# Optimization experiments

Measured on AMD Instinct MI355X. Metric: run time of the kernel, lower is better.

## Reference

```python
import jax, jax.numpy as jnp
import numpy as np

B, S, H, NH = 2, 2048, 1024, 16
HD = H // NH


def setup_inputs() -> dict:
    key = jax.random.key(0)
    ks = jax.random.split(key, 14)
    lim = 1.0 / np.sqrt(H)  # torch Linear default init range
    def lin(ka, kb):
        W = jax.random.uniform(ka, (H, H), jnp.float32, -lim, lim)
        b = jax.random.uniform(kb, (H,), jnp.float32, -lim, lim)
        return W, b
    Wq, bq = lin(ks[0], ks[1])
    Wk, bk = lin(ks[2], ks[3])
    Wv, bv = lin(ks[4], ks[5])
    Wo, bo = lin(ks[6], ks[7])
    return {
        "query": jax.random.normal(ks[8], (B, S, H), jnp.float32),
        "key": jax.random.normal(ks[9], (B, S, H), jnp.float32),
        "value": jax.random.normal(ks[10], (B, S, H), jnp.float32),
        "attn_mask": jax.random.randint(ks[11], (B, S, S), 0, 2).astype(bool),
        "relative_time": jax.random.normal(ks[12], (B, 1, S, S), jnp.float32),
        "Wq": Wq, "bq": bq, "Wk": Wk, "bk": bk,
        "Wv": Wv, "bv": bv, "Wo": Wo, "bo": bo,
    }


def reference(query, key, value, attn_mask, relative_time,
              Wq, bq, Wk, bk, Wv, bv, Wo, bo):
    Bq, Sq, _ = query.shape
    Skv = key.shape[1]
    # projections (torch Linear: x @ W^T + b)
    Q = (query @ Wq.T + bq).reshape(Bq, Sq, NH, HD).transpose(0, 2, 1, 3)
    K = (key @ Wk.T + bk).reshape(Bq, Skv, NH, HD).transpose(0, 2, 1, 3)
    V = (value @ Wv.T + bv).reshape(Bq, Skv, NH, HD).transpose(0, 2, 1, 3)
    scale = HD ** (-0.5)
    # NOTE: bias added BEFORE scaling, matching the original (non-standard)
    scores = jnp.einsum("bhqd,bhkd->bhqk", Q, K)
    scores = (scores + relative_time) * scale
    scores = jnp.where(attn_mask[:, None, :, :], scores, -jnp.inf)
    attn = jax.nn.softmax(scores.astype(jnp.float32), axis=-1).astype(scores.dtype)
    attn = jnp.nan_to_num(attn, nan=0.0)
    # dropout is identity in eval mode (dropout_rate applied only when training)
    out = jnp.einsum("bhqk,bhkd->bhqd", attn, V)
    out = out.transpose(0, 2, 1, 3).reshape(Bq, Sq, H)
    return out @ Wo.T + bo
```

## Files before the change

kernel.cpp:

```cpp
#include <hip/hip_runtime.h>
#include <hip/hip_bf16.h>

constexpr int BATCH = 2, SEQ = 2048, HDIM = 1024, NHEADS = 16, HEADD = 64;
constexpr int MROWS = BATCH * SEQ;
constexpr float QSCALE = 0.18033688011112042f;

typedef short short8  __attribute__((ext_vector_type(8)));
typedef float f32x4   __attribute__((ext_vector_type(4)));
typedef float f32x16  __attribute__((ext_vector_type(16)));
typedef int   int4v   __attribute__((ext_vector_type(4)));
typedef unsigned short ushort4v __attribute__((ext_vector_type(4)));

static __device__ __forceinline__ short f2bf(float f) {
    __hip_bfloat16 h = __float2bfloat16(f);
    return *reinterpret_cast<short*>(&h);
}

static __device__ __forceinline__ int cvt_pk_bf16(float a, float b) {
    int r;
    asm("v_cvt_pk_bf16_f32 %0, %1, %2" : "=v"(r) : "v"(a), "v"(b));
    return r;
}

static __device__ __forceinline__ float bfbits2f(unsigned short u) {
    return __builtin_bit_cast(float, (unsigned int)u << 16);
}

static __device__ __forceinline__ void gload_lds16(const void* g, void* l) {
    __builtin_amdgcn_global_load_lds(
        (const __attribute__((address_space(1))) unsigned int*)g,
        (__attribute__((address_space(3))) unsigned int*)l, 16, 0, 0);
}

static __device__ __forceinline__ int swz(int row) {
    return (((row & 7) ^ ((row >> 3) & 3))) << 4;
}

__global__ void cvt_all_kernel(const float* __restrict__ q, const float* __restrict__ k,
                               const float* __restrict__ v, const float* __restrict__ w0,
                               const float* __restrict__ w1, const float* __restrict__ w2,
                               const float* __restrict__ w3,
                               short* __restrict__ xq, short* __restrict__ xk,
                               short* __restrict__ xv, short* __restrict__ o0,
                               short* __restrict__ o1, short* __restrict__ o2,
                               short* __restrict__ o3, int n4x, int n4w) {
    int i = blockIdx.x * blockDim.x + threadIdx.x;
    const int stride = gridDim.x * blockDim.x;
    const int total = 3 * n4x + 4 * n4w;
    for (; i < total; i += stride) {
        const float* in; short* out; int j = i;
        if (j < 3 * n4x) {
            if (j >= 2 * n4x)      { in = v; out = xv; j -= 2 * n4x; }
            else if (j >= n4x)     { in = k; out = xk; j -= n4x; }
            else                   { in = q; out = xq; }
        } else {
            j -= 3 * n4x;
            if (j >= 3 * n4w)      { in = w3; out = o3; j -= 3 * n4w; }
            else if (j >= 2 * n4w) { in = w2; out = o2; j -= 2 * n4w; }
            else if (j >= n4w)     { in = w1; out = o1; j -= n4w; }
            else                   { in = w0; out = o0; }
        }
        const float4 val = reinterpret_cast<const float4*>(in)[j];
        short4 o;
        o.x = f2bf(val.x); o.y = f2bf(val.y); o.z = f2bf(val.z); o.w = f2bf(val.w);
        reinterpret_cast<short4*>(out)[j] = o;
    }
}

__global__ void detect_mask_kernel(const unsigned int* __restrict__ m, int* flag) {
    const int tid = threadIdx.x;
    int gt1 = 0, isf = 0;
    for (int i = 0; i < 4; ++i) {
        unsigned int wv = m[tid + 256 * i];
        if (wv > 1u) gt1 = 1;
        if (wv == 0x3F800000u) isf = 1;
    }
    __shared__ int s_gt1, s_isf;
    if (tid == 0) { s_gt1 = 0; s_isf = 0; }
    __syncthreads();
    if (gt1) atomicOr(&s_gt1, 1);
    if (isf) atomicOr(&s_isf, 1);
    __syncthreads();
    if (tid == 0) flag[0] = s_gt1 ? (s_isf ? 2 : 1) : 0;
}

__global__ __launch_bounds__(256)
void fuse_rel_kernel(const float* __restrict__ rel, const void* __restrict__ mask,
                     const int* __restrict__ flag, short* __restrict__ rT) {
    constexpr int QT = 64, KT = 256;
    constexpr int STRIDE = KT + 4;
    __shared__ short tile[QT * STRIDE];
    const int f   = flag[0];
    const int bid = blockIdx.x;
    const int b   = bid >> 8;
    const int t8  = (bid >> 5) & 7;
    const int t32 = bid & 31;
    const int q0  = t32 * QT;
    const int kv0 = t8 * KT;
    const int tid = threadIdx.x;

    const int c4 = tid & 63;
    const int r4 = tid >> 6;
    #pragma unroll 4
    for (int it = 0; it < 16; ++it) {
        const int row = it * 4 + r4;
        const long src = ((long)(b * 2048 + q0 + row)) * 2048 + kv0 + c4 * 4;
        const float4 v = *reinterpret_cast<const float4*>(rel + src);
        bool mk[4];
        if (f == 1) {
            const unsigned int mw =
                *reinterpret_cast<const unsigned int*>((const unsigned char*)mask + src);
            mk[0] = (mw & 0xffu) != 0;       mk[1] = (mw & 0xff00u) != 0;
            mk[2] = (mw & 0xff0000u) != 0;   mk[3] = (mw & 0xff000000u) != 0;
        } else if (f == 0) {
            const int4 mi = *reinterpret_cast<const int4*>((const int*)mask + src);
            mk[0] = mi.x != 0; mk[1] = mi.y != 0; mk[2] = mi.z != 0; mk[3] = mi.w != 0;
        } else {
            const float4 mf = *reinterpret_cast<const float4*>((const float*)mask + src);
            mk[0] = mf.x != 0.0f; mk[1] = mf.y != 0.0f;
            mk[2] = mf.z != 0.0f; mk[3] = mf.w != 0.0f;
        }
        short4 o;
        o.x = f2bf(mk[0] ? v.x * QSCALE : -1e30f);
        o.y = f2bf(mk[1] ? v.y * QSCALE : -1e30f);
        o.z = f2bf(mk[2] ? v.z * QSCALE : -1e30f);
        o.w = f2bf(mk[3] ? v.w * QSCALE : -1e30f);
        *reinterpret_cast<short4*>(&tile[row * STRIDE + c4 * 4]) = o;
    }
    __syncthreads();

    const int qq  = tid & 63;
    const int p4r = tid >> 6;
    #pragma unroll 4
    for (int it = 0; it < 16; ++it) {
        const int pl = it * 4 + p4r;
        const short4 o = *reinterpret_cast<const short4*>(&tile[qq * STRIDE + pl * 4]);
        *reinterpret_cast<short4*>(
            rT + (((long)(b * 512 + (kv0 >> 2) + pl)) * 2048 + q0 + qq) * 4) = o;
    }
}

template<int BN, typename EPI>
static __device__ __forceinline__
void gemm_core(const short* A, const short* Bw, int K, int m0, int n0, EPI epi) {
    constexpr int NFRAG = BN / 32;
    __shared__ short As[128 * 64];
    __shared__ short Bs[BN * 64];
    const int tid  = threadIdx.x;
    const int lane = tid & 63;
    const int w    = tid >> 6;
    const int lo   = lane & 15, hi = lane >> 4;
    const int wm   = w >> 1, wn = w & 1;

    f32x4 acc[4][NFRAG] = {};

    const int arow  = tid >> 3;
    const int acolb = (tid & 7) * 16;
    const int scolS = acolb ^ swz(arow);
    const char* Ab = (const char*)A + ((long)(m0 + arow) * K) * 2 + scolS;
    const char* Bb = (const char*)Bw + ((long)(n0 + arow) * K) * 2 + scolS;

    for (int k0 = 0; k0 < K; k0 += 64) {
        #pragma unroll
        for (int i = 0; i < 4; ++i)
            gload_lds16(Ab + ((long)i * 32 * K + k0) * 2, (char*)As + i * 4096 + tid * 16);
        #pragma unroll
        for (int i = 0; i < NFRAG; ++i)
            gload_lds16(Bb + ((long)i * 32 * K + k0) * 2, (char*)Bs + i * 4096 + tid * 16);
        __syncthreads();
        #pragma unroll
        for (int ks = 0; ks < 2; ++ks) {
            short8 af[4], bf[NFRAG];
            #pragma unroll
            for (int fm = 0; fm < 4; ++fm) {
                const int row = wm * 64 + fm * 16 + lo;
                af[fm] = *reinterpret_cast<const short8*>(
                    (const char*)As + row * 128 + ((ks * 64 + hi * 16) ^ swz(row)));
            }
            #pragma unroll
            for (int fn = 0; fn < NFRAG; ++fn) {
                const int row = wn * (BN / 2) + fn * 16 + lo;
                bf[fn] = *reinterpret_cast<const short8*>(
                    (const char*)Bs + row * 128 + ((ks * 64 + hi * 16) ^ swz(row)));
            }
            #pragma unroll
            for (int fm = 0; fm < 4; ++fm)
                #pragma unroll
                for (int fn = 0; fn < NFRAG; ++fn)
                    acc[fm][fn] = __builtin_amdgcn_mfma_f32_16x16x32_bf16(
                        af[fm], bf[fn], acc[fm][fn], 0, 0, 0);
        }
        __syncthreads();
    }

    #pragma unroll
    for (int fm = 0; fm < 4; ++fm)
        #pragma unroll
        for (int fn = 0; fn < NFRAG; ++fn) {
            const int n = n0 + wn * (BN / 2) + fn * 16 + lo;
            const int mB = m0 + wm * 64 + fm * 16 + hi * 4;
            for (int r = 0; r < 4; ++r) epi(mB + r, n, acc[fm][fn][r]);
        }
}

__global__ __launch_bounds__(256, 3)
void qkv_gemm(const short* xq, const short* xk, const short* xv,
              const short* wq, const short* wk, const short* wv,
              const float* bq, const float* bk, const float* bv,
              short* Qb, short* Kb, short* Vt) {
    const int which = blockIdx.x >> 8;
    const int bid   = blockIdx.x & 255;
    const int m0 = (bid >> 3) << 7;
    const int n0 = (bid & 7) << 7;
    const short* A    = which == 0 ? xq : which == 1 ? xk : xv;
    const short* W    = which == 0 ? wq : which == 1 ? wk : wv;
    const float* bias = which == 0 ? bq : which == 1 ? bk : bv;
    short* C          = which == 0 ? Qb : which == 1 ? Kb : Vt;
    const float scale = which == 0 ? QSCALE : 1.0f;
    gemm_core<128>(A, W, HDIM, m0, n0, [&](int m, int n, float v) {
        v = (v + bias[n]) * scale;
        const int b = m >> 11, s = m & (SEQ - 1);
        const int h = n >> 6, d = n & 63;
        long idx;
        if (which != 2) idx = (((long)(b * NHEADS + h)) * SEQ + s) * HEADD + d;
        else            idx = (((long)(b * NHEADS + h)) * HEADD + d) * SEQ + s;
        C[idx] = f2bf(v);
    });
}

__global__ __launch_bounds__(256, 2)
void out_gemm(const short* A, const short* W, const float* bias, float* Cout) {
    const int bid = blockIdx.x;
    const int m0 = (bid >> 4) << 7;
    const int n0 = (bid & 15) << 6;
    gemm_core<64>(A, W, HDIM, m0, n0, [&](int m, int n, float v) {
        Cout[(long)m * HDIM + n] = v + bias[n];
    });
}

__global__ __launch_bounds__(256, 4)
void attn_fwd(const short* __restrict__ Qb, const short* __restrict__ Kb,
              const short* __restrict__ Vtb, const short* __restrict__ rT,
              short* __restrict__ Ob) {
    __shared__ short Ks[2][64 * 64];
    __shared__ short Vs[2][64 * 64];
    const int tid  = threadIdx.x;
    const int lane = tid & 63;
    const int wv   = tid >> 6;
    const int qp   = wv & 1;
    const int t    = wv >> 1;
    const int l31  = lane & 31, hi2 = lane >> 5;
    const int wg = ((blockIdx.x & 7) << 7) + (blockIdx.x >> 3);
    const int qt = wg & 31, h = (wg >> 5) & 15, b = wg >> 9;
    const int bh = b * NHEADS + h;
    const int q0 = qt * 64 + qp * 32 + l31;

    short8 qf[4];
    {
        const short* qp_ = Qb + ((long)bh * SEQ + q0) * HEADD + hi2 * 8;
        #pragma unroll
        for (int s = 0; s < 4; ++s)
            qf[s] = *reinterpret_cast<const short8*>(qp_ + s * 16);
    }

    float lsum = 0.0f;
    f32x16 oacc0 = {}, oacc1 = {};

    const int srow  = tid >> 3;
    const int scolb = (tid & 7) * 16;
    const int scolK = scolb ^ swz(srow);
    const char* KbB = (const char*)Kb + ((long)bh * SEQ + srow) * 128 + scolK;
    const char* VbB = (const char*)Vtb + ((long)bh * HEADD + srow) * ((long)SEQ * 2) + scolK;

    auto stage = [&](int buf, int kt) {
        #pragma unroll
        for (int i = 0; i < 2; ++i) {
            gload_lds16(KbB + ((long)kt * 64 + i * 32) * 128,
                        (char*)&Ks[buf][0] + i * 4096 + tid * 16);
            gload_lds16(VbB + (long)i * 32 * (SEQ * 2) + (long)kt * 128,
                        (char*)&Vs[buf][0] + i * 4096 + tid * 16);
        }
    };

    ushort4v rbuf[4];
    auto loadRel = [&](int kt) {
        #pragma unroll
        for (int g = 0; g < 4; ++g) {
            const int p4 = kt * 16 + t * 8 + 2 * g + hi2;
            rbuf[g] = *reinterpret_cast<const ushort4v*>(
                rT + (((long)(b * 512 + p4)) * 2048 + q0) * 4);
        }
    };

    stage(0, 0);
    loadRel(0);

    const int rsw = swz(l31);
    const int NT = SEQ / 64;

    for (int kt = 0; kt < NT; ++kt) {
        const int cb = kt & 1;
        const bool hasNext = (kt < NT - 1);
        if (hasNext) stage(cb ^ 1, kt + 1);
        if (hasNext) asm volatile("s_waitcnt vmcnt(4)" ::: "memory");
        else         asm volatile("s_waitcnt vmcnt(0)" ::: "memory");
        __builtin_amdgcn_s_barrier();
        asm volatile("" ::: "memory");

        f32x16 sc;
        #pragma unroll
        for (int g = 0; g < 4; ++g)
            #pragma unroll
            for (int j = 0; j < 4; ++j)
                sc[4 * g + j] = bfbits2f(rbuf[g][j]);
        if (hasNext) loadRel(kt + 1);

        const char* kr = (const char*)&Ks[cb][0] + (t * 32 + l31) * 128;
        __builtin_amdgcn_s_setprio(1);
        #pragma unroll
        for (int s = 0; s < 4; ++s) {
            short8 kf = *reinterpret_cast<const short8*>(kr + ((s * 32 + hi2 * 16) ^ rsw));
            sc = __builtin_amdgcn_mfma_f32_32x32x16_bf16(kf, qf[s], sc, 0, 0, 0);
        }
        __builtin_amdgcn_s_setprio(0);

        int X[8];
        #pragma unroll
        for (int i2 = 0; i2 < 8; ++i2) {
            const float p0 = __builtin_amdgcn_exp2f(sc[2 * i2]);
            const float p1 = __builtin_amdgcn_exp2f(sc[2 * i2 + 1]);
            lsum += p0 + p1;
            X[i2] = cvt_pk_bf16(p0, p1);
        }
        int pa[2][4];
        #pragma unroll
        for (int u = 0; u < 2; ++u) {
            auto r0 = __builtin_amdgcn_permlane32_swap(X[4 * u + 0], X[4 * u + 2], false, false);
            auto r1 = __builtin_amdgcn_permlane32_swap(X[4 * u + 1], X[4 * u + 3], false, false);
            pa[u][0] = (int)r0[0];
            pa[u][1] = (int)r1[0];
            pa[u][2] = (int)r0[1];
            pa[u][3] = (int)r1[1];
        }

        const char* vls = (const char*)&Vs[cb][0];
        __builtin_amdgcn_s_setprio(1);
        #pragma unroll
        for (int dt = 0; dt < 2; ++dt) {
            const char* vr = vls + (dt * 32 + l31) * 128;
            #pragma unroll
            for (int u = 0; u < 2; ++u) {
                const int s = 2 * t + u;
                short8 vf = *reinterpret_cast<const short8*>(vr + ((s * 32 + hi2 * 16) ^ rsw));
                int4v pw = { pa[u][0], pa[u][1], pa[u][2], pa[u][3] };
                if (dt == 0)
                    oacc0 = __builtin_amdgcn_mfma_f32_32x32x16_bf16(
                        __builtin_bit_cast(short8, pw), vf, oacc0, 0, 0, 0);
                else
                    oacc1 = __builtin_amdgcn_mfma_f32_32x32x16_bf16(
                        __builtin_bit_cast(short8, pw), vf, oacc1, 0, 0, 0);
            }
        }
        __builtin_amdgcn_s_setprio(0);

        asm volatile("" ::: "memory");
        __builtin_amdgcn_s_barrier();
    }

    lsum += __shfl_xor(lsum, 32, 64);

    float* cmbO = (float*)&Ks[0][0];
    float* cmbL = (float*)&Vs[0][0];
    if (t == 1) {
        #pragma unroll
        for (int r = 0; r < 16; ++r) {
            const int qloc = (r & 3) + 8 * (r >> 2) + 4 * hi2;
            cmbO[(qp * 32 + qloc) * 64 + l31]      = oacc0[r];
            cmbO[(qp * 32 + qloc) * 64 + 32 + l31] = oacc1[r];
        }
        if (hi2 == 0) cmbL[qp * 32 + l31] = lsum;
    }
    __syncthreads();
    if (t == 0) {
        const float ltot = lsum + cmbL[qp * 32 + l31];
        const float inv  = ltot > 0.0f ? 1.0f / ltot : 0.0f;
        #pragma unroll
        for (int r = 0; r < 16; ++r) {
            const int qloc = (r & 3) + 8 * (r >> 2) + 4 * hi2;
            const float invr = __shfl(inv, qloc, 64);
            const int qg = qt * 64 + qp * 32 + qloc;
            const long obase = ((long)b * SEQ + qg) * HDIM + h * 64 + l31;
            const float o0 = oacc0[r] + cmbO[(qp * 32 + qloc) * 64 + l31];
            const float o1 = oacc1[r] + cmbO[(qp * 32 + qloc) * 64 + 32 + l31];
            Ob[obase]      = f2bf(o0 * invr);
            Ob[obase + 32] = f2bf(o1 * invr);
        }
    }
}

extern "C" void kernel_launch(void* const* d_in, const int* in_sizes, int n_in,
                              void* d_out, int out_size, void* d_ws, size_t ws_size,
                              hipStream_t stream) {
    const float* q    = (const float*)d_in[0];
    const float* k    = (const float*)d_in[1];
    const float* v    = (const float*)d_in[2];
    const void*  mask = d_in[3];
    const float* rel  = (const float*)d_in[4];
    const float* Wq   = (const float*)d_in[5];
    const float* bq   = (const float*)d_in[6];
    const float* Wk   = (const float*)d_in[7];
    const float* bk   = (const float*)d_in[8];
    const float* Wv   = (const float*)d_in[9];
    const float* bv   = (const float*)d_in[10];
    const float* Wo   = (const float*)d_in[11];
    const float* bo   = (const float*)d_in[12];
    (void)in_sizes; (void)n_in; (void)out_size; (void)ws_size;

    char* ws = (char*)d_ws;
    size_t off = 0;
    auto alloc = [&](size_t bytes) {
        char* p = ws + off;
        off += (bytes + 255) & ~(size_t)255;
        return p;
    };
    const size_t xBytes = (size_t)MROWS * HDIM * 2;
    const size_t wBytes = (size_t)HDIM * HDIM * 2;
    const size_t poolBytes = 3 * xBytes + 3 * wBytes;

    short* Qb  = (short*)alloc(xBytes);
    short* Kb  = (short*)alloc(xBytes);
    short* Vt  = (short*)alloc(xBytes);
    short* wob = (short*)alloc(wBytes);
    int*   flag = (int*)alloc(256);
    char* pool = (char*)alloc(poolBytes);
    short* Ab  = (short*)alloc(xBytes);

    short* xq  = (short*)(pool);
    short* xk  = (short*)(pool + xBytes);
    short* xv  = (short*)(pool + 2 * xBytes);
    short* wqb = (short*)(pool + 3 * xBytes);
    short* wkb = (short*)(pool + 3 * xBytes + wBytes);
    short* wvb = (short*)(pool + 3 * xBytes + 2 * wBytes);
    short* rT  = (short*)(pool);

    const int n4x = MROWS * HDIM / 4, n4w = HDIM * HDIM / 4;
    cvt_all_kernel<<<2048, 256, 0, stream>>>(q, k, v, Wq, Wk, Wv, Wo,
                                             xq, xk, xv, wqb, wkb, wvb, wob, n4x, n4w);
    detect_mask_kernel<<<1, 256, 0, stream>>>((const unsigned int*)mask, flag);

    qkv_gemm<<<768, 256, 0, stream>>>(xq, xk, xv, wqb, wkb, wvb,
                                      bq, bk, bv, Qb, Kb, Vt);

    fuse_rel_kernel<<<512, 256, 0, stream>>>(rel, mask, flag, rT);

    attn_fwd<<<1024, 256, 0, stream>>>(Qb, Kb, Vt, rT, Ab);

    out_gemm<<<512, 256, 0, stream>>>(Ab, wob, bo, (float*)d_out);
}
```

Baseline: 156.2 us.

## Merge QKV GEMM and relative-bias/mask prep into one interleaved launch

Gives the bias/mask fusion kernel its own workspace buffer so it no longer aliases the bf16 input pool. QKV GEMM blocks and rel-fusion blocks are then interleaved in a single 1280-block launch, three GEMM tiles to every two rel tiles. The goal is to overlap the memory-bound rel transpose with the compute-bound GEMM and drop one kernel boundary. The cost is extra workspace plus a fallback path when the workspace is too small, and shared-memory sizing is unified at 16640 shorts, which may affect occupancy.

```diff
diff --git a/kernel.cpp b/kernel.cpp
--- a/kernel.cpp
+++ b/kernel.cpp
@@ -84,14 +84,11 @@
     if (tid == 0) flag[0] = s_gt1 ? (s_isf ? 2 : 1) : 0;
 }
 
-__global__ __launch_bounds__(256)
-void fuse_rel_kernel(const float* __restrict__ rel, const void* __restrict__ mask,
-                     const int* __restrict__ flag, short* __restrict__ rT) {
+static __device__ __forceinline__
+void fuse_rel_body(short* tile, int bid, const float* __restrict__ rel,
+                   const void* __restrict__ mask, int f, short* __restrict__ rT) {
     constexpr int QT = 64, KT = 256;
     constexpr int STRIDE = KT + 4;
-    __shared__ short tile[QT * STRIDE];
-    const int f   = flag[0];
-    const int bid = blockIdx.x;
     const int b   = bid >> 8;
     const int t8  = (bid >> 5) & 7;
     const int t32 = bid & 31;
@@ -140,12 +137,19 @@
     }
 }
 
+__global__ __launch_bounds__(256)
+void fuse_rel_kernel(const float* __restrict__ rel, const void* __restrict__ mask,
+                     const int* __restrict__ flag, short* __restrict__ rT) {
+    __shared__ short tile[16640];
+    fuse_rel_body(tile, blockIdx.x, rel, mask, flag[0], rT);
+}
+
 template<int BN, typename EPI>
 static __device__ __forceinline__
-void gemm_core(const short* A, const short* Bw, int K, int m0, int n0, EPI epi) {
+void gemm_core(short* smem, const short* A, const short* Bw, int K, int m0, int n0, EPI epi) {
     constexpr int NFRAG = BN / 32;
-    __shared__ short As[128 * 64];
-    __shared__ short Bs[BN * 64];
+    short* As = smem;
+    short* Bs = smem + 128 * 64;
     const int tid  = threadIdx.x;
     const int lane = tid & 63;
     const int w    = tid >> 6;
@@ -203,13 +207,14 @@
         }
 }
 
-__global__ __launch_bounds__(256, 3)
-void qkv_gemm(const short* xq, const short* xk, const short* xv,
+static __device__ __forceinline__
+void qkv_body(short* smem, int qb,
+              const short* xq, const short* xk, const short* xv,
               const short* wq, const short* wk, const short* wv,
               const float* bq, const float* bk, const float* bv,
               short* Qb, short* Kb, short* Vt) {
-    const int which = blockIdx.x >> 8;
-    const int bid   = blockIdx.x & 255;
+    const int which = qb >> 8;
+    const int bid   = qb & 255;
     const int m0 = (bid >> 3) << 7;
     const int n0 = (bid & 7) << 7;
     const short* A    = which == 0 ? xq : which == 1 ? xk : xv;
@@ -217,7 +222,7 @@
     const float* bias = which == 0 ? bq : which == 1 ? bk : bv;
     short* C          = which == 0 ? Qb : which == 1 ? Kb : Vt;
     const float scale = which == 0 ? QSCALE : 1.0f;
-    gemm_core<128>(A, W, HDIM, m0, n0, [&](int m, int n, float v) {
+    gemm_core<128>(smem, A, W, HDIM, m0, n0, [&](int m, int n, float v) {
         v = (v + bias[n]) * scale;
         const int b = m >> 11, s = m & (SEQ - 1);
         const int h = n >> 6, d = n & 63;
@@ -228,12 +233,38 @@
     });
 }
 
+__global__ __launch_bounds__(256, 3)
+void qkv_gemm(const short* xq, const short* xk, const short* xv,
+              const short* wq, const short* wk, const short* wv,
+              const float* bq, const float* bk, const float* bv,
+              short* Qb, short* Kb, short* Vt) {
+    __shared__ short smem[16640];
+    qkv_body(smem, blockIdx.x, xq, xk, xv, wq, wk, wv, bq, bk, bv, Qb, Kb, Vt);
+}
+
+__global__ __launch_bounds__(256, 3)
+void qkv_rel_kernel(const short* xq, const short* xk, const short* xv,
+                    const short* wq, const short* wk, const short* wv,
+                    const float* bq, const float* bk, const float* bv,
+                    short* Qb, short* Kb, short* Vt,
+                    const float* rel, const void* mask, const int* flag, short* rT) {
+    __shared__ short smem[16640];
+    const int r = blockIdx.x % 5;
+    const int g = blockIdx.x / 5;
+    if (r < 3) {
+        qkv_body(smem, g * 3 + r, xq, xk, xv, wq, wk, wv, bq, bk, bv, Qb, Kb, Vt);
+    } else {
+        fuse_rel_body(smem, g * 2 + (r - 3), rel, mask, flag[0], rT);
+    }
+}
+
 __global__ __launch_bounds__(256, 2)
 void out_gemm(const short* A, const short* W, const float* bias, float* Cout) {
+    __shared__ short smem[(128 + 64) * 64];
     const int bid = blockIdx.x;
     const int m0 = (bid >> 4) << 7;
     const int n0 = (bid & 15) << 6;
-    gemm_core<64>(A, W, HDIM, m0, n0, [&](int m, int n, float v) {
+    gemm_core<64>(smem, A, W, HDIM, m0, n0, [&](int m, int n, float v) {
         Cout[(long)m * HDIM + n] = v + bias[n];
     });
 }
@@ -414,7 +445,7 @@
     const float* bv   = (const float*)d_in[10];
     const float* Wo   = (const float*)d_in[11];
     const float* bo   = (const float*)d_in[12];
-    (void)in_sizes; (void)n_in; (void)out_size; (void)ws_size;
+    (void)in_sizes; (void)n_in; (void)out_size;
 
     char* ws = (char*)d_ws;
     size_t off = 0;
@@ -423,16 +454,17 @@
         off += (bytes + 255) & ~(size_t)255;
         return p;
     };
-    const size_t xBytes = (size_t)MROWS * HDIM * 2;
-    const size_t wBytes = (size_t)HDIM * HDIM * 2;
+    const size_t xBytes  = (size_t)MROWS * HDIM * 2;
+    const size_t wBytes  = (size_t)HDIM * HDIM * 2;
     const size_t poolBytes = 3 * xBytes + 3 * wBytes;
+    const size_t rtBytes = (size_t)BATCH * 2048 * 2048 * 2;
 
     short* Qb  = (short*)alloc(xBytes);
     short* Kb  = (short*)alloc(xBytes);
     short* Vt  = (short*)alloc(xBytes);
     short* wob = (short*)alloc(wBytes);
     int*   flag = (int*)alloc(256);
-    char* pool = (char*)alloc(poolBytes);
+    char*  pool = (char*)alloc(poolBytes);
     short* Ab  = (short*)alloc(xBytes);
 
     short* xq  = (short*)(pool);
@@ -441,17 +473,24 @@
     short* wqb = (short*)(pool + 3 * xBytes);
     short* wkb = (short*)(pool + 3 * xBytes + wBytes);
     short* wvb = (short*)(pool + 3 * xBytes + 2 * wBytes);
-    short* rT  = (short*)(pool);
+
+    const bool fused = (off + rtBytes + 256) <= ws_size;
+    short* rT = fused ? (short*)alloc(rtBytes) : (short*)pool;
 
     const int n4x = MROWS * HDIM / 4, n4w = HDIM * HDIM / 4;
     cvt_all_kernel<<<2048, 256, 0, stream>>>(q, k, v, Wq, Wk, Wv, Wo,
                                              xq, xk, xv, wqb, wkb, wvb, wob, n4x, n4w);
     detect_mask_kernel<<<1, 256, 0, stream>>>((const unsigned int*)mask, flag);
 
-    qkv_gemm<<<768, 256, 0, stream>>>(xq, xk, xv, wqb, wkb, wvb,
-                                      bq, bk, bv, Qb, Kb, Vt);
-
-    fuse_rel_kernel<<<512, 256, 0, stream>>>(rel, mask, flag, rT);
+    if (fused) {
+        qkv_rel_kernel<<<1280, 256, 0, stream>>>(xq, xk, xv, wqb, wkb, wvb,
+                                                 bq, bk, bv, Qb, Kb, Vt,
+                                                 rel, mask, flag, rT);
+    } else {
+        qkv_gemm<<<768, 256, 0, stream>>>(xq, xk, xv, wqb, wkb, wvb,
+                                          bq, bk, bv, Qb, Kb, Vt);
+        fuse_rel_kernel<<<512, 256, 0, stream>>>(rel, mask, flag, rT);
+    }
 
     attn_fwd<<<1024, 256, 0, stream>>>(Qb, Kb, Vt, rT, Ab);
 
```

Result: slower. 166.8 us (+6.7%).
